# Optimization experiments

Measured on AMD Instinct MI355X. Metric: run time of the kernel, lower is better.

## Reference

```python
import jax, jax.numpy as jnp
import numpy as np

COMMITMENT_COST = 0.25


def setup_inputs() -> dict:
    key = jax.random.key(0)
    k1, k2 = jax.random.split(key)
    z = jax.random.normal(k1, (16, 1024, 256), dtype=jnp.float32)
    embedding = jax.random.normal(k2, (8192, 256), dtype=jnp.float32)
    return {"z": z, "embedding": embedding}


def reference(z, embedding):
    B, N, C = z.shape
    flat = z.reshape(-1, C)  # (B*N, C)
    d = (
        jnp.sum(flat * flat, axis=1, keepdims=True)
        + jnp.sum(embedding * embedding, axis=1)
        - 2.0 * jnp.matmul(flat, embedding.T)
    )  # (B*N, K)
    idx = jnp.argmin(d, axis=1)  # (B*N,)
    quantized = jnp.take(embedding, idx, axis=0).reshape(B, N, C)
    # losses (matching torch detach semantics; in eval fwd-only these are plain MSEs)
    e_latent_loss = jnp.mean((jax.lax.stop_gradient(quantized) - z) ** 2)
    q_latent_loss = jnp.mean((quantized - jax.lax.stop_gradient(z)) ** 2)
    vq_loss = q_latent_loss + COMMITMENT_COST * e_latent_loss
    # straight-through estimator
    quantized_ste = z + jax.lax.stop_gradient(quantized - z)
    encoding_indices = idx.reshape(B, N)
    return quantized_ste, vq_loss, encoding_indices
```

## Files before the change

kernel.cpp:

```cpp
#include <hip/hip_runtime.h>
#include <math.h>

#define MROWS   16384
#define KCODES  8192
#define CDIM    256

#define LOSS_OFF 4194304
#define IDXOFF   4194305

#define NSPLIT  8
#define WS_EF   0
#define WS_ZF   (WS_EF + KCODES * CDIM * 2)
#define WS_EN   (WS_ZF + MROWS * CDIM * 2)
#define WS_PI   (WS_EN + KCODES * 4)

#define CODES_PER_SPLIT (KCODES / NSPLIT)
#define STEPS (CODES_PER_SPLIT / 16)

typedef float    v4f __attribute__((ext_vector_type(4)));
typedef _Float16 v8h __attribute__((ext_vector_type(8)));
typedef __attribute__((address_space(1))) const unsigned int gu32;
typedef __attribute__((address_space(3))) unsigned int su32;

__global__ void conv_kernel(const float* __restrict__ z,
                            const float* __restrict__ emb,
                            char* __restrict__ ws,
                            float* __restrict__ loss_slot) {
    int t = blockIdx.x * 256 + threadIdx.x;
    const int NZ = MROWS * 32;
    const float4* s4;
    _Float16* dst;
    int j, c;
    bool isE = (t >= NZ);
    if (!isE) {
        j = t >> 5; c = t & 31;
        s4 = (const float4*)(z + (size_t)j * CDIM) + c * 2;
        dst = (_Float16*)(ws + WS_ZF);
    } else {
        int u = t - NZ;
        j = u >> 5; c = u & 31;
        s4 = (const float4*)(emb + (size_t)j * CDIM) + c * 2;
        dst = (_Float16*)(ws + WS_EF);
    }
    float4 a = s4[0], b = s4[1];
    v8h h;
    h[0] = (_Float16)a.x; h[1] = (_Float16)a.y;
    h[2] = (_Float16)a.z; h[3] = (_Float16)a.w;
    h[4] = (_Float16)b.x; h[5] = (_Float16)b.y;
    h[6] = (_Float16)b.z; h[7] = (_Float16)b.w;
    *(v8h*)(dst + ((size_t)(j >> 4) * 32 + c) * 128 + (j & 15) * 8) = h;
    if (isE) {
        float s = a.x * a.x + a.y * a.y + a.z * a.z + a.w * a.w +
                  b.x * b.x + b.y * b.y + b.z * b.z + b.w * b.w;
#pragma unroll
        for (int m = 1; m <= 16; m <<= 1) s += __shfl_xor(s, m, 64);
        if (c == 0) ((float*)(ws + WS_EN))[j] = s + 1024.0f;
    }
    if (t == 0) *loss_slot = 0.f;
}

__global__ __launch_bounds__(256, 2)
void vq_pass1_kernel(const char* __restrict__ ws_c, char* __restrict__ ws) {
    __shared__ __attribute__((aligned(16))) char bbuf[2][8192];
    int tid  = threadIdx.x;
    int lane = tid & 63;
    int w    = tid >> 6;
    int tm   = lane & 15;
    int q    = lane >> 4;

    int b  = blockIdx.x;
    int sp = b & 7;
    int rb = b >> 3;
    int r0 = rb * 256 + w * 64;

    const _Float16* zf_g = (const _Float16*)(ws_c + WS_ZF);
    v8h zf[4][8];
#pragma unroll
    for (int mi = 0; mi < 4; ++mi) {
        const _Float16* zr = zf_g + (size_t)((r0 >> 4) + mi) * 4096 + q * 128 + tm * 8;
#pragma unroll
        for (int kc = 0; kc < 8; ++kc)
            zf[mi][kc] = *(const v8h*)(zr + kc * 512);
    }

    const char*  efb  = ws_c + WS_EF + (size_t)(sp * 64) * 8192;
    const float* en_g = (const float*)(ws_c + WS_EN);

#define STAGE(st, bi) do {                                                      \
        const char* g0 = efb + (size_t)(st) * 8192 + w * 2048 + lane * 16;      \
        char* l0 = &bbuf[bi][w * 2048];                                         \
        __builtin_amdgcn_global_load_lds((gu32*)g0, (su32*)l0, 16, 0, 0);       \
        __builtin_amdgcn_global_load_lds((gu32*)(g0 + 1024),                    \
                                         (su32*)(l0 + 1024), 16, 0, 0);         \
    } while (0)

    unsigned rk[16];
#pragma unroll
    for (int s = 0; s < 16; ++s) rk[s] = 0xFFFFFFFFu;

    STAGE(0, 0);
    float enr = en_g[sp * 1024 + tm];
    __syncthreads();

#pragma unroll 1
    for (int st = 0; st < STEPS; ++st) {
        int cur = st & 1;
        if (st < STEPS - 1) STAGE(st + 1, cur ^ 1);

        const char* lb = &bbuf[cur][q * 256 + tm * 16];
        v8h bf[8];
#pragma unroll
        for (int kc = 0; kc < 8; ++kc) bf[kc] = *(const v8h*)(lb + kc * 1024);
        float enn = (st < STEPS - 1) ? en_g[sp * 1024 + (st + 1) * 16 + tm] : enr;

        v4f acc[4];
#pragma unroll
        for (int mi = 0; mi < 4; ++mi)
            acc[mi] = __builtin_amdgcn_mfma_f32_16x16x32_f16(zf[mi][0], bf[0], (v4f)0.f, 0, 0, 0);
#pragma unroll
        for (int kc = 1; kc < 8; ++kc)
#pragma unroll
            for (int mi = 0; mi < 4; ++mi)
                acc[mi] = __builtin_amdgcn_mfma_f32_16x16x32_f16(zf[mi][kc], bf[kc], acc[mi], 0, 0, 0);

#pragma unroll
        for (int mi = 0; mi < 4; ++mi)
#pragma unroll
            for (int r = 0; r < 4; ++r) {
                float s = fmaf(-2.f, acc[mi][r], enr);
                unsigned key = (__float_as_uint(s) << 6) | (unsigned)st;
                int slot = mi * 4 + r;
                rk[slot] = key < rk[slot] ? key : rk[slot];
            }
        enr = enn;
        __syncthreads();
    }
#undef STAGE

#pragma unroll
    for (int slot = 0; slot < 16; ++slot) {
        unsigned k = rk[slot];
        int      t_ = tm;
#pragma unroll
        for (int m = 1; m <= 8; m <<= 1) {
            unsigned k2 = __shfl_xor(k, m, 64);
            int      t2 = __shfl_xor(t_, m, 64);
            if (k2 < k || (k2 == k && t2 < t_)) { k = k2; t_ = t2; }
        }
        if (tm == 0) {
            int row = r0 + (slot >> 2) * 16 + q * 4 + (slot & 3);
            int bi  = sp * 1024 + (int)(k & 63u) * 16 + t_;
            ((int*)(ws + WS_PI))[sp * MROWS + row] = bi;
        }
    }
}

__global__ void rerank_out_kernel(const float* __restrict__ z,
                                  const float* __restrict__ emb,
                                  const char* __restrict__ ws,
                                  float* __restrict__ out) {
    __shared__ float wsum[4];
    const int* pi = (const int*)(ws + WS_PI);
    int tid = threadIdx.x, lane = tid & 63, w = tid >> 6;
    int g = lane >> 3, sub = lane & 7;
    const float4* e4 = (const float4*)emb;
    const float4* z4 = (const float4*)z;
    float lsum = 0.f;

#pragma unroll 1
    for (int it = 0; it < 4; ++it) {
        int row = it * 4096 + blockIdx.x * 4 + w;
        int ci = pi[g * MROWS + row];
        float s = 0.f;
#pragma unroll
        for (int j = 0; j < 8; ++j) {
            float4 ev = e4[(size_t)ci * 64 + sub * 8 + j];
            float4 zv = z4[(size_t)row * 64 + sub * 8 + j];
            float dx = ev.x - zv.x, dy = ev.y - zv.y;
            float dz = ev.z - zv.z, dw = ev.w - zv.w;
            s += dx * dx + dy * dy + dz * dz + dw * dw;
        }
#pragma unroll
        for (int m = 1; m <= 4; m <<= 1) s += __shfl_xor(s, m, 64);
        float dv = s; int di = ci;
#pragma unroll
        for (int m = 8; m <= 32; m <<= 1) {
            float d2 = __shfl_xor(dv, m, 64);
            int   i2 = __shfl_xor(di, m, 64);
            if (d2 < dv || (d2 == dv && i2 < di)) { dv = d2; di = i2; }
        }
        if (lane == 0) out[IDXOFF + row] = (float)di;
        float4 qv = e4[(size_t)di * 64 + lane];
        float4 zv = z4[(size_t)row * 64 + lane];
        float dx = qv.x - zv.x, dy = qv.y - zv.y;
        float dz = qv.z - zv.z, dw = qv.w - zv.w;
        float4 o;
        o.x = zv.x + dx; o.y = zv.y + dy; o.z = zv.z + dz; o.w = zv.w + dw;
        ((float4*)out)[(size_t)row * 64 + lane] = o;
        lsum += dx * dx + dy * dy + dz * dz + dw * dw;
    }

#pragma unroll
    for (int m = 32; m >= 1; m >>= 1) lsum += __shfl_xor(lsum, m, 64);
    if (lane == 0) wsum[w] = lsum;
    __syncthreads();
    if (tid == 0)
        atomicAdd(out + LOSS_OFF,
                  (wsum[0] + wsum[1] + wsum[2] + wsum[3]) * (1.25f / 4194304.f));
}

extern "C" void kernel_launch(void* const* d_in, const int* in_sizes, int n_in,
                              void* d_out, int out_size, void* d_ws, size_t ws_size,
                              hipStream_t stream) {
    const float* z   = (const float*)d_in[0];
    const float* emb = (const float*)d_in[1];
    float* out = (float*)d_out;
    char*  ws  = (char*)d_ws;

    hipLaunchKernelGGL(conv_kernel, dim3((MROWS + KCODES) * 32 / 256), dim3(256),
                       0, stream, z, emb, ws, out + LOSS_OFF);
    hipLaunchKernelGGL(vq_pass1_kernel, dim3((MROWS / 256) * NSPLIT), dim3(256),
                       0, stream, ws, ws);
    hipLaunchKernelGGL(rerank_out_kernel, dim3(1024), dim3(256),
                       0, stream, z, emb, ws, out);
}
```

Before: 188.5 us.

## Stage 32 codes per step and prune rerank candidates by approximate distance

The pass1 loop now stages 32 codebook entries per iteration with a larger LDS double buffer, halving barrier and loop overhead. Pass1 also stores each split's approximate best distance, and rerank skips exact fp32 distance computation for candidates whose approximate distance exceeds the group minimum by more than a fixed margin. This cuts embedding loads in rerank but relies on the fp16 error staying under the margin, which risks wrong indices in near-tie cases. Doubling LDS use may also affect occupancy.

```diff
diff --git a/kernel.cpp b/kernel.cpp
--- a/kernel.cpp
+++ b/kernel.cpp
@@ -13,9 +13,10 @@
 #define WS_ZF   (WS_EF + KCODES * CDIM * 2)
 #define WS_EN   (WS_ZF + MROWS * CDIM * 2)
 #define WS_PI   (WS_EN + KCODES * 4)
+#define WS_PD   (WS_PI + NSPLIT * MROWS * 4)
 
 #define CODES_PER_SPLIT (KCODES / NSPLIT)
-#define STEPS (CODES_PER_SPLIT / 16)
+#define STEPS32 (CODES_PER_SPLIT / 32)
 
 typedef float    v4f __attribute__((ext_vector_type(4)));
 typedef _Float16 v8h __attribute__((ext_vector_type(8)));
@@ -61,7 +62,7 @@
 
 __global__ __launch_bounds__(256, 2)
 void vq_pass1_kernel(const char* __restrict__ ws_c, char* __restrict__ ws) {
-    __shared__ __attribute__((aligned(16))) char bbuf[2][8192];
+    __shared__ __attribute__((aligned(16))) char bbuf[2][16384];
     int tid  = threadIdx.x;
     int lane = tid & 63;
     int w    = tid >> 6;
@@ -87,11 +88,15 @@
     const float* en_g = (const float*)(ws_c + WS_EN);
 
 #define STAGE(st, bi) do {                                                      \
-        const char* g0 = efb + (size_t)(st) * 8192 + w * 2048 + lane * 16;      \
-        char* l0 = &bbuf[bi][w * 2048];                                         \
+        const char* g0 = efb + (size_t)(st) * 16384 + w * 4096 + lane * 16;     \
+        char* l0 = &bbuf[bi][w * 4096];                                         \
         __builtin_amdgcn_global_load_lds((gu32*)g0, (su32*)l0, 16, 0, 0);       \
         __builtin_amdgcn_global_load_lds((gu32*)(g0 + 1024),                    \
                                          (su32*)(l0 + 1024), 16, 0, 0);         \
+        __builtin_amdgcn_global_load_lds((gu32*)(g0 + 2048),                    \
+                                         (su32*)(l0 + 2048), 16, 0, 0);         \
+        __builtin_amdgcn_global_load_lds((gu32*)(g0 + 3072),                    \
+                                         (su32*)(l0 + 3072), 16, 0, 0);         \
     } while (0)
 
     unsigned rk[16];
@@ -99,40 +104,48 @@
     for (int s = 0; s < 16; ++s) rk[s] = 0xFFFFFFFFu;
 
     STAGE(0, 0);
-    float enr = en_g[sp * 1024 + tm];
+    float enr0 = en_g[sp * 1024 + tm];
+    float enr1 = en_g[sp * 1024 + 16 + tm];
     __syncthreads();
 
 #pragma unroll 1
-    for (int st = 0; st < STEPS; ++st) {
+    for (int st = 0; st < STEPS32; ++st) {
         int cur = st & 1;
-        if (st < STEPS - 1) STAGE(st + 1, cur ^ 1);
-
-        const char* lb = &bbuf[cur][q * 256 + tm * 16];
-        v8h bf[8];
-#pragma unroll
-        for (int kc = 0; kc < 8; ++kc) bf[kc] = *(const v8h*)(lb + kc * 1024);
-        float enn = (st < STEPS - 1) ? en_g[sp * 1024 + (st + 1) * 16 + tm] : enr;
-
-        v4f acc[4];
-#pragma unroll
-        for (int mi = 0; mi < 4; ++mi)
-            acc[mi] = __builtin_amdgcn_mfma_f32_16x16x32_f16(zf[mi][0], bf[0], (v4f)0.f, 0, 0, 0);
-#pragma unroll
-        for (int kc = 1; kc < 8; ++kc)
+        if (st < STEPS32 - 1) STAGE(st + 1, cur ^ 1);
+        int stn = (st < STEPS32 - 1) ? st + 1 : st;
+        float enn0 = en_g[sp * 1024 + stn * 32 + tm];
+        float enn1 = en_g[sp * 1024 + stn * 32 + 16 + tm];
+
+#pragma unroll
+        for (int ct = 0; ct < 2; ++ct) {
+            const char* lb = &bbuf[cur][ct * 8192 + q * 256 + tm * 16];
+            v8h bf[8];
+#pragma unroll
+            for (int kc = 0; kc < 8; ++kc) bf[kc] = *(const v8h*)(lb + kc * 1024);
+
+            v4f acc[4];
 #pragma unroll
             for (int mi = 0; mi < 4; ++mi)
-                acc[mi] = __builtin_amdgcn_mfma_f32_16x16x32_f16(zf[mi][kc], bf[kc], acc[mi], 0, 0, 0);
-
-#pragma unroll
-        for (int mi = 0; mi < 4; ++mi)
-#pragma unroll
-            for (int r = 0; r < 4; ++r) {
-                float s = fmaf(-2.f, acc[mi][r], enr);
-                unsigned key = (__float_as_uint(s) << 6) | (unsigned)st;
-                int slot = mi * 4 + r;
-                rk[slot] = key < rk[slot] ? key : rk[slot];
-            }
-        enr = enn;
+                acc[mi] = __builtin_amdgcn_mfma_f32_16x16x32_f16(zf[mi][0], bf[0], (v4f)0.f, 0, 0, 0);
+#pragma unroll
+            for (int kc = 1; kc < 8; ++kc)
+#pragma unroll
+                for (int mi = 0; mi < 4; ++mi)
+                    acc[mi] = __builtin_amdgcn_mfma_f32_16x16x32_f16(zf[mi][kc], bf[kc], acc[mi], 0, 0, 0);
+
+            float enc = ct ? enr1 : enr0;
+            unsigned tag = (unsigned)(st * 2 + ct);
+#pragma unroll
+            for (int mi = 0; mi < 4; ++mi)
+#pragma unroll
+                for (int r = 0; r < 4; ++r) {
+                    float s = fmaf(-2.f, acc[mi][r], enc);
+                    unsigned key = (__float_as_uint(s) << 6) | tag;
+                    int slot = mi * 4 + r;
+                    rk[slot] = key < rk[slot] ? key : rk[slot];
+                }
+        }
+        enr0 = enn0; enr1 = enn1;
         __syncthreads();
     }
 #undef STAGE
@@ -151,6 +164,8 @@
             int row = r0 + (slot >> 2) * 16 + q * 4 + (slot & 3);
             int bi  = sp * 1024 + (int)(k & 63u) * 16 + t_;
             ((int*)(ws + WS_PI))[sp * MROWS + row] = bi;
+            ((float*)(ws + WS_PD))[sp * MROWS + row] =
+                __uint_as_float((k >> 6) | (17u << 26));
         }
     }
 }
@@ -160,7 +175,8 @@
                                   const char* __restrict__ ws,
                                   float* __restrict__ out) {
     __shared__ float wsum[4];
-    const int* pi = (const int*)(ws + WS_PI);
+    const int*   pi = (const int*)(ws + WS_PI);
+    const float* pd = (const float*)(ws + WS_PD);
     int tid = threadIdx.x, lane = tid & 63, w = tid >> 6;
     int g = lane >> 3, sub = lane & 7;
     const float4* e4 = (const float4*)emb;
@@ -170,15 +186,24 @@
 #pragma unroll 1
     for (int it = 0; it < 4; ++it) {
         int row = it * 4096 + blockIdx.x * 4 + w;
-        int ci = pi[g * MROWS + row];
-        float s = 0.f;
-#pragma unroll
-        for (int j = 0; j < 8; ++j) {
-            float4 ev = e4[(size_t)ci * 64 + sub * 8 + j];
-            float4 zv = z4[(size_t)row * 64 + sub * 8 + j];
-            float dx = ev.x - zv.x, dy = ev.y - zv.y;
-            float dz = ev.z - zv.z, dw = ev.w - zv.w;
-            s += dx * dx + dy * dy + dz * dz + dw * dw;
+        int ci   = pi[g * MROWS + row];
+        float pg = pd[g * MROWS + row];
+        float dmin = pg;
+#pragma unroll
+        for (int m = 8; m <= 32; m <<= 1) dmin = fminf(dmin, __shfl_xor(dmin, m, 64));
+        float s;
+        if (pg <= dmin + 0.75f) {
+            s = 0.f;
+#pragma unroll
+            for (int j = 0; j < 8; ++j) {
+                float4 ev = e4[(size_t)ci * 64 + sub * 8 + j];
+                float4 zv = z4[(size_t)row * 64 + sub * 8 + j];
+                float dx = ev.x - zv.x, dy = ev.y - zv.y;
+                float dz = ev.z - zv.z, dw = ev.w - zv.w;
+                s += dx * dx + dy * dy + dz * dz + dw * dw;
+            }
+        } else {
+            s = 3e38f;
         }
 #pragma unroll
         for (int m = 1; m <= 4; m <<= 1) s += __shfl_xor(s, m, 64);
```

New measurement: 168.5 us. -10.6%, faster.
